# Optimization experiments

Measured on AMD Instinct MI355X. Metric: run time of the kernel, lower is better.

The kernel has to match this reference:

```python
import jax, jax.numpy as jnp
import numpy as np
import math

N, T, D, H = 64, 512, 1024, 1024

def setup_inputs() -> dict:
    key = jax.random.key(0)
    k1, k2, k3, k4 = jax.random.split(key, 4)
    x = jax.random.normal(k1, (N, T, D), dtype=jnp.float32)
    h0 = jax.random.normal(k2, (N, H), dtype=jnp.float32)
    Wx = jax.random.normal(k3, (D, 4 * H), dtype=jnp.float32) / math.sqrt(D)
    Wh = jax.random.normal(k4, (H, 4 * H), dtype=jnp.float32) / math.sqrt(H)
    b = jnp.zeros((4 * H,), dtype=jnp.float32)
    return {"x": x, "h0": h0, "Wx": Wx, "Wh": Wh, "b": b}

def reference(x, h0, Wx, Wh, b):
    Hdim = h0.shape[1]
    c0 = jnp.zeros_like(h0)
    # Precompute input projection for all timesteps: [N,T,4H] -> time-major [T,N,4H]
    xW = jnp.einsum('ntd,dk->tnk', x, Wx) + b

    def step(carry, xw_t):
        prev_h, prev_c = carry
        a = xw_t + prev_h @ Wh  # [N, 4H]
        i = jax.nn.sigmoid(a[:, :Hdim])
        f = jax.nn.sigmoid(a[:, Hdim:2 * Hdim])
        o = jax.nn.sigmoid(a[:, 2 * Hdim:3 * Hdim])
        g = jnp.tanh(a[:, 3 * Hdim:])
        next_c = f * prev_c + i * g
        next_h = o * jnp.tanh(next_c)
        return (next_h, next_c), next_h

    _, hs = jax.lax.scan(step, (h0, c0), xW)  # hs: [T, N, H]
    return jnp.transpose(hs, (1, 0, 2))  # [N, T, H]
```

## Files before the change

kernel.cpp:

```cpp
#include <hip/hip_runtime.h>

typedef short bf16x8 __attribute__((ext_vector_type(8)));
typedef float f32x4 __attribute__((ext_vector_type(4)));

static constexpr int kT = 512;
static constexpr int kN = 64;
static constexpr int kD = 1024;
static constexpr int kH = 1024;
static constexpr int kG = 4 * kH;

__device__ __forceinline__ unsigned short f2bf(float f) {
  unsigned u = __builtin_bit_cast(unsigned, f);
  return (unsigned short)((u + 0x7fffu + ((u >> 16) & 1u)) >> 16);
}
__device__ __forceinline__ unsigned pack2(float a, float b) {
  return (unsigned)f2bf(a) | ((unsigned)f2bf(b) << 16);
}
__device__ __forceinline__ float fsigmoid(float v) {
  return __builtin_amdgcn_rcpf(1.0f + __expf(-v));
}
__device__ __forceinline__ float ftanh(float v) {
  return 1.0f - 2.0f * __builtin_amdgcn_rcpf(__expf(2.0f * v) + 1.0f);
}

__device__ __forceinline__ bf16x8 gld16_coh(unsigned long long a) {
  bf16x8 r;
  asm volatile("global_load_dwordx4 %0, %1, off sc0 sc1" : "=v"(r) : "v"(a) : "memory");
  return r;
}
__device__ __forceinline__ bf16x8 gld16(unsigned long long a) {
  bf16x8 r;
  asm volatile("global_load_dwordx4 %0, %1, off" : "=v"(r) : "v"(a) : "memory");
  return r;
}

__global__ __launch_bounds__(256) void xconv(const float* __restrict__ x,
                                             unsigned short* __restrict__ xbf) {
  const int gid = blockIdx.x * 256 + threadIdx.x;
  const float4* x4 = (const float4*)x;
  uint4* o = (uint4*)xbf;
  for (int i = gid; i < (kN * kT * kD) / 8; i += 2048 * 256) {
    const float4 f0 = x4[2 * i];
    const float4 f1 = x4[2 * i + 1];
    uint4 p;
    p.x = pack2(f0.x, f0.y); p.y = pack2(f0.z, f0.w);
    p.z = pack2(f1.x, f1.y); p.w = pack2(f1.z, f1.w);
    o[i] = p;
  }
}

template <bool PRE>
__global__ __launch_bounds__(256, 1)
void lstm_fg(const float* __restrict__ x, const float* __restrict__ h0,
             const float* __restrict__ Wx, const float* __restrict__ Wh,
             const float* __restrict__ bias, float* __restrict__ out,
             unsigned short* __restrict__ hbuf, unsigned* __restrict__ flags,
             const unsigned short* __restrict__ xbf) {
  __shared__ float ps[2][16 * 320];

  const int tid = threadIdx.x;
  const int bx = blockIdx.x;
  const int dom = (bx & 7) >> 1;
  const int ug = ((bx >> 3) << 1) | (bx & 1);
  const int wv = tid >> 6;
  const int lane = tid & 63;

  const int colc = ug * 16 + (lane & 15);
  const int krow = (lane >> 4) * 8;
  const int kb = wv * 256;
  bf16x8 wxf[4][8], whf[4][8];
#pragma unroll
  for (int ct = 0; ct < 4; ++ct) {
#pragma unroll
    for (int ks = 0; ks < 8; ++ks) {
      bf16x8 vx, vh;
#pragma unroll
      for (int e = 0; e < 8; ++e) {
        const size_t k = (size_t)(kb + ks * 32 + krow + e);
        vx[e] = (short)f2bf(Wx[k * kG + ct * kH + colc]);
        vh[e] = (short)f2bf(Wh[k * kG + ct * kH + colc]);
      }
      wxf[ct][ks] = vx;
      whf[ct][ks] = vh;
    }
  }

  const int n_l = tid >> 4;
  const int j_l = tid & 15;
  const int jg = ug * 16 + j_l;
  const float b_i = bias[jg];
  const float b_f = bias[kH + jg];
  const float b_o = bias[2 * kH + jg];
  const float b_g = bias[3 * kH + jg];
  float c = 0.0f;

  const int arow = lane & 15;
  const int nrow = dom * 16 + arow;
  const unsigned long long xbase0 =
      (unsigned long long)nrow * kT * kD * 2 + (unsigned long long)(kb + krow) * 2;
  const unsigned long long hbase0 =
      (unsigned long long)nrow * kH * 2 + (unsigned long long)(kb + krow) * 2;
  const unsigned pubeidx = (unsigned)((dom * 16 + n_l) * kH + jg);

  unsigned* myflag = flags + (dom * 256 + ug * 4 + wv);
  unsigned* pollp = flags + (dom * 256 + wv * 64 + lane);

  bf16x8 xfrag[8], hfrag[8];

  if (PRE) {
    const unsigned long long xb = (unsigned long long)xbf + xbase0;
#pragma unroll
    for (int ks = 0; ks < 8; ++ks) xfrag[ks] = gld16(xb + (unsigned)(ks * 64));
    asm volatile("s_waitcnt vmcnt(0)" ::: "memory");
    __builtin_amdgcn_sched_barrier(0);
  } else {
    const float* xr = x + (size_t)nrow * kT * kD + (kb + krow);
#pragma unroll
    for (int ks = 0; ks < 8; ++ks) {
      const float4 f0 = *(const float4*)(xr + ks * 32);
      const float4 f1 = *(const float4*)(xr + ks * 32 + 4);
      bf16x8 v;
      v[0] = (short)f2bf(f0.x); v[1] = (short)f2bf(f0.y);
      v[2] = (short)f2bf(f0.z); v[3] = (short)f2bf(f0.w);
      v[4] = (short)f2bf(f1.x); v[5] = (short)f2bf(f1.y);
      v[6] = (short)f2bf(f1.z); v[7] = (short)f2bf(f1.w);
      xfrag[ks] = v;
    }
  }
  f32x4 acc[4];
#pragma unroll
  for (int ct = 0; ct < 4; ++ct) acc[ct] = (f32x4){0.f, 0.f, 0.f, 0.f};
#pragma unroll
  for (int ks = 0; ks < 8; ++ks)
#pragma unroll
    for (int ct = 0; ct < 4; ++ct)
      acc[ct] = __builtin_amdgcn_mfma_f32_16x16x32_bf16(xfrag[ks], wxf[ct][ks], acc[ct], 0, 0, 0);
  {
    const float* hr = h0 + (size_t)nrow * kH + (kb + krow);
#pragma unroll
    for (int ks = 0; ks < 8; ++ks) {
      const float4 f0 = *(const float4*)(hr + ks * 32);
      const float4 f1 = *(const float4*)(hr + ks * 32 + 4);
      bf16x8 v;
      v[0] = (short)f2bf(f0.x); v[1] = (short)f2bf(f0.y);
      v[2] = (short)f2bf(f0.z); v[3] = (short)f2bf(f0.w);
      v[4] = (short)f2bf(f1.x); v[5] = (short)f2bf(f1.y);
      v[6] = (short)f2bf(f1.z); v[7] = (short)f2bf(f1.w);
      hfrag[ks] = v;
    }
  }

  for (int t = 0; t < kT; ++t) {
    asm volatile("s_waitcnt vmcnt(4)" ::: "memory");
    __builtin_amdgcn_sched_barrier(0);
#pragma unroll
    for (int ks = 0; ks < 4; ++ks)
#pragma unroll
      for (int ct = 0; ct < 4; ++ct)
        acc[ct] = __builtin_amdgcn_mfma_f32_16x16x32_bf16(hfrag[ks], whf[ct][ks], acc[ct], 0, 0, 0);
    asm volatile("s_waitcnt vmcnt(0)" ::: "memory");
    __builtin_amdgcn_sched_barrier(0);
#pragma unroll
    for (int ks = 4; ks < 8; ++ks)
#pragma unroll
      for (int ct = 0; ct < 4; ++ct)
        acc[ct] = __builtin_amdgcn_mfma_f32_16x16x32_bf16(hfrag[ks], whf[ct][ks], acc[ct], 0, 0, 0);

    float* p = ps[t & 1];
#pragma unroll
    for (int ct = 0; ct < 4; ++ct)
      *(f32x4*)&p[(ct * 4 + wv) * 320 + (lane & 15) * 20 + (lane >> 4) * 4] = acc[ct];
    __syncthreads();

    float a4[4];
#pragma unroll
    for (int g = 0; g < 4; ++g) {
      a4[g] = p[(g * 4 + 0) * 320 + j_l * 20 + n_l]
            + p[(g * 4 + 1) * 320 + j_l * 20 + n_l]
            + p[(g * 4 + 2) * 320 + j_l * 20 + n_l]
            + p[(g * 4 + 3) * 320 + j_l * 20 + n_l];
    }
    const float gi = fsigmoid(a4[0] + b_i);
    const float gf = fsigmoid(a4[1] + b_f);
    const float go = fsigmoid(a4[2] + b_o);
    const float gg = ftanh(a4[3] + b_g);
    c = gf * c + gi * gg;
    const float hv = go * ftanh(c);

    if (t < kT - 1) {
      const unsigned tgt = (unsigned)(t + 1);
      const unsigned buf1 = tgt & 1;
      const unsigned mybf = (unsigned)f2bf(hv);
      const unsigned up = (unsigned)__shfl_xor((int)mybf, 1);
      if ((j_l & 1) == 0) {
        __hip_atomic_store((unsigned*)(hbuf + buf1 * (kN * kH) + pubeidx),
                           mybf | (up << 16), __ATOMIC_RELAXED, __HIP_MEMORY_SCOPE_AGENT);
      }
      asm volatile("s_waitcnt vmcnt(0)" ::: "memory");
      __builtin_amdgcn_sched_barrier(0);
      if (lane == 0)
        __hip_atomic_store(myflag, tgt, __ATOMIC_RELAXED, __HIP_MEMORY_SCOPE_AGENT);

      __builtin_nontemporal_store(hv, &out[((size_t)(dom * 16 + n_l) * kT + t) * kH + jg]);

      if (PRE) {
        const unsigned long long xb = (unsigned long long)xbf + xbase0 +
                                      (unsigned long long)(t + 1) * 2048u;
#pragma unroll
        for (int ks = 0; ks < 8; ++ks) xfrag[ks] = gld16(xb + (unsigned)(ks * 64));
        asm volatile("s_waitcnt vmcnt(0)" ::: "memory");
        __builtin_amdgcn_sched_barrier(0);
      } else {
        const float* xr = x + (size_t)nrow * kT * kD + (size_t)(t + 1) * kD + (kb + krow);
#pragma unroll
        for (int ks = 0; ks < 8; ++ks) {
          const float4 f0 = *(const float4*)(xr + ks * 32);
          const float4 f1 = *(const float4*)(xr + ks * 32 + 4);
          bf16x8 v;
          v[0] = (short)f2bf(f0.x); v[1] = (short)f2bf(f0.y);
          v[2] = (short)f2bf(f0.z); v[3] = (short)f2bf(f0.w);
          v[4] = (short)f2bf(f1.x); v[5] = (short)f2bf(f1.y);
          v[6] = (short)f2bf(f1.z); v[7] = (short)f2bf(f1.w);
          xfrag[ks] = v;
        }
      }
#pragma unroll
      for (int ct = 0; ct < 4; ++ct) acc[ct] = (f32x4){0.f, 0.f, 0.f, 0.f};
#pragma unroll
      for (int ks = 0; ks < 8; ++ks)
#pragma unroll
        for (int ct = 0; ct < 4; ++ct)
          acc[ct] = __builtin_amdgcn_mfma_f32_16x16x32_bf16(xfrag[ks], wxf[ct][ks], acc[ct], 0, 0, 0);

      for (;;) {
        const unsigned v = __hip_atomic_load(pollp, __ATOMIC_RELAXED,
                                             __HIP_MEMORY_SCOPE_AGENT);
        if (__all((int)v >= (int)tgt)) break;
        __builtin_amdgcn_s_sleep(1);
      }
      __builtin_amdgcn_sched_barrier(0);

      const unsigned long long hb = (unsigned long long)hbuf +
                                    (unsigned long long)buf1 * (kN * kH * 2) + hbase0;
#pragma unroll
      for (int ks = 0; ks < 8; ++ks) hfrag[ks] = gld16_coh(hb + (unsigned)(ks * 64));
    } else {
      __builtin_nontemporal_store(hv, &out[((size_t)(dom * 16 + n_l) * kT + t) * kH + jg]);
    }
  }
}

extern "C" void kernel_launch(void* const* d_in, const int* in_sizes, int n_in,
                              void* d_out, int out_size, void* d_ws, size_t ws_size,
                              hipStream_t stream) {
  (void)in_sizes; (void)n_in; (void)out_size;
  const float* x  = (const float*)d_in[0];
  const float* h0 = (const float*)d_in[1];
  const float* Wx = (const float*)d_in[2];
  const float* Wh = (const float*)d_in[3];
  const float* b  = (const float*)d_in[4];
  float* out = (float*)d_out;

  const size_t o_hbuf = 4096;
  const size_t o_xbf = o_hbuf + 262144;
  const size_t need_pre = o_xbf + (size_t)kN * kT * kD * 2;

  unsigned* flags = (unsigned*)d_ws;
  unsigned short* hbuf = (unsigned short*)((char*)d_ws + o_hbuf);
  unsigned short* xbf = (unsigned short*)((char*)d_ws + o_xbf);

  hipMemsetAsync(d_ws, 0, 4096, stream);

  if (ws_size >= need_pre) {
    hipLaunchKernelGGL(xconv, dim3(2048), dim3(256), 0, stream, x, xbf);
    hipLaunchKernelGGL(HIP_KERNEL_NAME(lstm_fg<true>), dim3(256), dim3(256), 0, stream,
                       x, h0, Wx, Wh, b, out, hbuf, flags, xbf);
  } else {
    hipLaunchKernelGGL(HIP_KERNEL_NAME(lstm_fg<false>), dim3(256), dim3(256), 0, stream,
                       x, h0, Wx, Wh, b, out, hbuf, flags,
                       (const unsigned short*)nullptr);
  }
}
```

Baseline: 2.011 ms.

## Replace flag-then-load handoff with timestep-tagged hidden-state words polled directly

Each published hidden value is now stored as a 32-bit word holding the timestep tag in the upper half and the bf16 value in the lower half. Consumers poll the data words themselves, removing the serial flag-poll-then-load round trip per step. The old flag path is kept as a fallback after a bounded number of polling attempts. This doubles hidden-state buffer traffic, issues 64 scalar atomic loads per lane per poll, and moves the flag store after the x prefetch.

After: 4.990 ms. 148% more time.

```diff
diff --git a/kernel.cpp b/kernel.cpp
--- a/kernel.cpp
+++ b/kernel.cpp
@@ -23,8 +23,8 @@
   return 1.0f - 2.0f * __builtin_amdgcn_rcpf(__expf(2.0f * v) + 1.0f);
 }
 
-__device__ __forceinline__ bf16x8 gld16_coh(unsigned long long a) {
-  bf16x8 r;
+__device__ __forceinline__ uint4 gld16_coh_u(unsigned long long a) {
+  uint4 r;
   asm volatile("global_load_dwordx4 %0, %1, off sc0 sc1" : "=v"(r) : "v"(a) : "memory");
   return r;
 }
@@ -51,10 +51,10 @@
 
 template <bool PRE>
 __global__ __launch_bounds__(256, 1)
-void lstm_fg(const float* __restrict__ x, const float* __restrict__ h0,
+void lstm_tf(const float* __restrict__ x, const float* __restrict__ h0,
              const float* __restrict__ Wx, const float* __restrict__ Wh,
              const float* __restrict__ bias, float* __restrict__ out,
-             unsigned short* __restrict__ hbuf, unsigned* __restrict__ flags,
+             unsigned* __restrict__ hTag, unsigned* __restrict__ flags,
              const unsigned short* __restrict__ xbf) {
   __shared__ float ps[2][16 * 320];
 
@@ -98,8 +98,7 @@
   const int nrow = dom * 16 + arow;
   const unsigned long long xbase0 =
       (unsigned long long)nrow * kT * kD * 2 + (unsigned long long)(kb + krow) * 2;
-  const unsigned long long hbase0 =
-      (unsigned long long)nrow * kH * 2 + (unsigned long long)(kb + krow) * 2;
+  const unsigned hrowelem = (unsigned)(nrow * kH + kb + krow);
   const unsigned pubeidx = (unsigned)((dom * 16 + n_l) * kH + jg);
 
   unsigned* myflag = flags + (dom * 256 + ug * 4 + wv);
@@ -151,17 +150,8 @@
   }
 
   for (int t = 0; t < kT; ++t) {
-    asm volatile("s_waitcnt vmcnt(4)" ::: "memory");
-    __builtin_amdgcn_sched_barrier(0);
-#pragma unroll
-    for (int ks = 0; ks < 4; ++ks)
-#pragma unroll
-      for (int ct = 0; ct < 4; ++ct)
-        acc[ct] = __builtin_amdgcn_mfma_f32_16x16x32_bf16(hfrag[ks], whf[ct][ks], acc[ct], 0, 0, 0);
-    asm volatile("s_waitcnt vmcnt(0)" ::: "memory");
-    __builtin_amdgcn_sched_barrier(0);
-#pragma unroll
-    for (int ks = 4; ks < 8; ++ks)
+#pragma unroll
+    for (int ks = 0; ks < 8; ++ks)
 #pragma unroll
       for (int ct = 0; ct < 4; ++ct)
         acc[ct] = __builtin_amdgcn_mfma_f32_16x16x32_bf16(hfrag[ks], whf[ct][ks], acc[ct], 0, 0, 0);
@@ -189,27 +179,16 @@
 
     if (t < kT - 1) {
       const unsigned tgt = (unsigned)(t + 1);
-      const unsigned buf1 = tgt & 1;
-      const unsigned mybf = (unsigned)f2bf(hv);
-      const unsigned up = (unsigned)__shfl_xor((int)mybf, 1);
-      if ((j_l & 1) == 0) {
-        __hip_atomic_store((unsigned*)(hbuf + buf1 * (kN * kH) + pubeidx),
-                           mybf | (up << 16), __ATOMIC_RELAXED, __HIP_MEMORY_SCOPE_AGENT);
-      }
-      asm volatile("s_waitcnt vmcnt(0)" ::: "memory");
-      __builtin_amdgcn_sched_barrier(0);
-      if (lane == 0)
-        __hip_atomic_store(myflag, tgt, __ATOMIC_RELAXED, __HIP_MEMORY_SCOPE_AGENT);
-
-      __builtin_nontemporal_store(hv, &out[((size_t)(dom * 16 + n_l) * kT + t) * kH + jg]);
+      unsigned* tbuf = hTag + (tgt & 1) * (unsigned)(kN * kH);
+
+      __hip_atomic_store(tbuf + pubeidx, (tgt << 16) | (unsigned)f2bf(hv),
+                         __ATOMIC_RELAXED, __HIP_MEMORY_SCOPE_AGENT);
 
       if (PRE) {
         const unsigned long long xb = (unsigned long long)xbf + xbase0 +
                                       (unsigned long long)(t + 1) * 2048u;
 #pragma unroll
         for (int ks = 0; ks < 8; ++ks) xfrag[ks] = gld16(xb + (unsigned)(ks * 64));
-        asm volatile("s_waitcnt vmcnt(0)" ::: "memory");
-        __builtin_amdgcn_sched_barrier(0);
       } else {
         const float* xr = x + (size_t)nrow * kT * kD + (size_t)(t + 1) * kD + (kb + krow);
 #pragma unroll
@@ -224,6 +203,13 @@
           xfrag[ks] = v;
         }
       }
+      asm volatile("s_waitcnt vmcnt(0)" ::: "memory");
+      __builtin_amdgcn_sched_barrier(0);
+      if (lane == 0)
+        __hip_atomic_store(myflag, tgt, __ATOMIC_RELAXED, __HIP_MEMORY_SCOPE_AGENT);
+
+      __builtin_nontemporal_store(hv, &out[((size_t)(dom * 16 + n_l) * kT + t) * kH + jg]);
+
 #pragma unroll
       for (int ct = 0; ct < 4; ++ct) acc[ct] = (f32x4){0.f, 0.f, 0.f, 0.f};
 #pragma unroll
@@ -232,18 +218,62 @@
         for (int ct = 0; ct < 4; ++ct)
           acc[ct] = __builtin_amdgcn_mfma_f32_16x16x32_bf16(xfrag[ks], wxf[ct][ks], acc[ct], 0, 0, 0);
 
-      for (;;) {
-        const unsigned v = __hip_atomic_load(pollp, __ATOMIC_RELAXED,
-                                             __HIP_MEMORY_SCOPE_AGENT);
-        if (__all((int)v >= (int)tgt)) break;
+      const unsigned* pb = tbuf + hrowelem;
+      unsigned tgv[8][8];
+      bool got = false;
+#pragma unroll 1
+      for (int it = 0; it < 24; ++it) {
+        unsigned bad = 0;
+#pragma unroll
+        for (int ks = 0; ks < 8; ++ks)
+#pragma unroll
+          for (int e = 0; e < 8; ++e) {
+            tgv[ks][e] = __hip_atomic_load(pb + ks * 32 + e, __ATOMIC_RELAXED,
+                                           __HIP_MEMORY_SCOPE_AGENT);
+            bad |= (tgv[ks][e] >> 16) ^ tgt;
+          }
+        if (__all(bad == 0)) { got = true; break; }
         __builtin_amdgcn_s_sleep(1);
       }
-      __builtin_amdgcn_sched_barrier(0);
-
-      const unsigned long long hb = (unsigned long long)hbuf +
-                                    (unsigned long long)buf1 * (kN * kH * 2) + hbase0;
-#pragma unroll
-      for (int ks = 0; ks < 8; ++ks) hfrag[ks] = gld16_coh(hb + (unsigned)(ks * 64));
+
+      if (got) {
+#pragma unroll
+        for (int ks = 0; ks < 8; ++ks) {
+          uint4 w;
+          w.x = (tgv[ks][0] & 0xFFFFu) | (tgv[ks][1] << 16);
+          w.y = (tgv[ks][2] & 0xFFFFu) | (tgv[ks][3] << 16);
+          w.z = (tgv[ks][4] & 0xFFFFu) | (tgv[ks][5] << 16);
+          w.w = (tgv[ks][6] & 0xFFFFu) | (tgv[ks][7] << 16);
+          hfrag[ks] = __builtin_bit_cast(bf16x8, w);
+        }
+      } else {
+        for (;;) {
+          const unsigned v = __hip_atomic_load(pollp, __ATOMIC_RELAXED,
+                                               __HIP_MEMORY_SCOPE_AGENT);
+          if (__all((int)v >= (int)tgt)) break;
+          __builtin_amdgcn_s_sleep(1);
+        }
+        __builtin_amdgcn_sched_barrier(0);
+        const unsigned long long hb = (unsigned long long)(tbuf + hrowelem);
+        uint4 tg4[16];
+#pragma unroll
+        for (int ks = 0; ks < 8; ++ks) {
+          tg4[2 * ks] = gld16_coh_u(hb + (unsigned)(ks * 128));
+          tg4[2 * ks + 1] = gld16_coh_u(hb + (unsigned)(ks * 128 + 16));
+        }
+        asm volatile("s_waitcnt vmcnt(0)" ::: "memory");
+        __builtin_amdgcn_sched_barrier(0);
+#pragma unroll
+        for (int ks = 0; ks < 8; ++ks) {
+          const uint4 a = tg4[2 * ks], b2 = tg4[2 * ks + 1];
+          uint4 w;
+          w.x = (a.x & 0xFFFFu) | (a.y << 16);
+          w.y = (a.z & 0xFFFFu) | (a.w << 16);
+          w.z = (b2.x & 0xFFFFu) | (b2.y << 16);
+          w.w = (b2.z & 0xFFFFu) | (b2.w << 16);
+          hfrag[ks] = __builtin_bit_cast(bf16x8, w);
+        }
+      }
     } else {
       __builtin_nontemporal_store(hv, &out[((size_t)(dom * 16 + n_l) * kT + t) * kH + jg]);
     }
@@ -261,23 +291,23 @@
   const float* b  = (const float*)d_in[4];
   float* out = (float*)d_out;
 
-  const size_t o_hbuf = 4096;
-  const size_t o_xbf = o_hbuf + 262144;
+  const size_t o_htag = 4096;
+  const size_t o_xbf = o_htag + 524288;
   const size_t need_pre = o_xbf + (size_t)kN * kT * kD * 2;
 
   unsigned* flags = (unsigned*)d_ws;
-  unsigned short* hbuf = (unsigned short*)((char*)d_ws + o_hbuf);
+  unsigned* hTag = (unsigned*)((char*)d_ws + o_htag);
   unsigned short* xbf = (unsigned short*)((char*)d_ws + o_xbf);
 
-  hipMemsetAsync(d_ws, 0, 4096, stream);
+  hipMemsetAsync(d_ws, 0, o_xbf, stream);
 
   if (ws_size >= need_pre) {
     hipLaunchKernelGGL(xconv, dim3(2048), dim3(256), 0, stream, x, xbf);
-    hipLaunchKernelGGL(HIP_KERNEL_NAME(lstm_fg<true>), dim3(256), dim3(256), 0, stream,
-                       x, h0, Wx, Wh, b, out, hbuf, flags, xbf);
+    hipLaunchKernelGGL(HIP_KERNEL_NAME(lstm_tf<true>), dim3(256), dim3(256), 0, stream,
+                       x, h0, Wx, Wh, b, out, hTag, flags, xbf);
   } else {
-    hipLaunchKernelGGL(HIP_KERNEL_NAME(lstm_fg<false>), dim3(256), dim3(256), 0, stream,
-                       x, h0, Wx, Wh, b, out, hbuf, flags,
+    hipLaunchKernelGGL(HIP_KERNEL_NAME(lstm_tf<false>), dim3(256), dim3(256), 0, stream,
+                       x, h0, Wx, Wh, b, out, hTag, flags,
                        (const unsigned short*)nullptr);
   }
 }
```

## Aggregate per-wave flags into one per-workgroup flag and pipeline h loads finer

Applied to the files above, without the earlier changes.

Each wave now bumps a shared-memory counter, and only the last wave of the workgroup publishes the step flag. This cuts the flag array from per-wave to per-workgroup entries, so pollers read 16 flags instead of 64. The wait on the hidden-state loads is split into four stages (vmcnt 6/4/2/0), letting MFMAs start as soon as each pair of fragments arrives. The flag publish now also waits for the x prefetch loads to finish, which may delay signalling. The unbounded shared counter relies on wave ordering across steps.

Result: slower. 2.688 ms (+33.7%).

```diff
diff --git a/kernel.cpp b/kernel.cpp
--- a/kernel.cpp
+++ b/kernel.cpp
@@ -33,6 +33,9 @@
   asm volatile("global_load_dwordx4 %0, %1, off" : "=v"(r) : "v"(a) : "memory");
   return r;
 }
+
+#define VMCNT(n) do { asm volatile("s_waitcnt vmcnt(" #n ")" ::: "memory"); \
+                      __builtin_amdgcn_sched_barrier(0); } while (0)
 
 __global__ __launch_bounds__(256) void xconv(const float* __restrict__ x,
                                              unsigned short* __restrict__ xbf) {
@@ -51,12 +54,13 @@
 
 template <bool PRE>
 __global__ __launch_bounds__(256, 1)
-void lstm_fg(const float* __restrict__ x, const float* __restrict__ h0,
-             const float* __restrict__ Wx, const float* __restrict__ Wh,
-             const float* __restrict__ bias, float* __restrict__ out,
-             unsigned short* __restrict__ hbuf, unsigned* __restrict__ flags,
-             const unsigned short* __restrict__ xbf) {
+void lstm_fg2(const float* __restrict__ x, const float* __restrict__ h0,
+              const float* __restrict__ Wx, const float* __restrict__ Wh,
+              const float* __restrict__ bias, float* __restrict__ out,
+              unsigned short* __restrict__ hbuf, unsigned* __restrict__ flags,
+              const unsigned short* __restrict__ xbf) {
   __shared__ float ps[2][16 * 320];
+  __shared__ unsigned wgcnt;
 
   const int tid = threadIdx.x;
   const int bx = blockIdx.x;
@@ -64,6 +68,8 @@
   const int ug = ((bx >> 3) << 1) | (bx & 1);
   const int wv = tid >> 6;
   const int lane = tid & 63;
+
+  if (tid == 0) wgcnt = 0;
 
   const int colc = ug * 16 + (lane & 15);
   const int krow = (lane >> 4) * 8;
@@ -102,8 +108,8 @@
       (unsigned long long)nrow * kH * 2 + (unsigned long long)(kb + krow) * 2;
   const unsigned pubeidx = (unsigned)((dom * 16 + n_l) * kH + jg);
 
-  unsigned* myflag = flags + (dom * 256 + ug * 4 + wv);
-  unsigned* pollp = flags + (dom * 256 + wv * 64 + lane);
+  unsigned* myflag = flags + (dom * 64 + ug);
+  unsigned* pollp = flags + (dom * 64 + wv * 16 + (lane & 15));
 
   bf16x8 xfrag[8], hfrag[8];
 
@@ -111,8 +117,7 @@
     const unsigned long long xb = (unsigned long long)xbf + xbase0;
 #pragma unroll
     for (int ks = 0; ks < 8; ++ks) xfrag[ks] = gld16(xb + (unsigned)(ks * 64));
-    asm volatile("s_waitcnt vmcnt(0)" ::: "memory");
-    __builtin_amdgcn_sched_barrier(0);
+    VMCNT(0);
   } else {
     const float* xr = x + (size_t)nrow * kT * kD + (kb + krow);
 #pragma unroll
@@ -149,19 +154,30 @@
       hfrag[ks] = v;
     }
   }
+  VMCNT(0);
 
   for (int t = 0; t < kT; ++t) {
-    asm volatile("s_waitcnt vmcnt(4)" ::: "memory");
-    __builtin_amdgcn_sched_barrier(0);
-#pragma unroll
-    for (int ks = 0; ks < 4; ++ks)
+    VMCNT(6);
+#pragma unroll
+    for (int ks = 0; ks < 2; ++ks)
 #pragma unroll
       for (int ct = 0; ct < 4; ++ct)
         acc[ct] = __builtin_amdgcn_mfma_f32_16x16x32_bf16(hfrag[ks], whf[ct][ks], acc[ct], 0, 0, 0);
-    asm volatile("s_waitcnt vmcnt(0)" ::: "memory");
-    __builtin_amdgcn_sched_barrier(0);
-#pragma unroll
-    for (int ks = 4; ks < 8; ++ks)
+    VMCNT(4);
+#pragma unroll
+    for (int ks = 2; ks < 4; ++ks)
+#pragma unroll
+      for (int ct = 0; ct < 4; ++ct)
+        acc[ct] = __builtin_amdgcn_mfma_f32_16x16x32_bf16(hfrag[ks], whf[ct][ks], acc[ct], 0, 0, 0);
+    VMCNT(2);
+#pragma unroll
+    for (int ks = 4; ks < 6; ++ks)
+#pragma unroll
+      for (int ct = 0; ct < 4; ++ct)
+        acc[ct] = __builtin_amdgcn_mfma_f32_16x16x32_bf16(hfrag[ks], whf[ct][ks], acc[ct], 0, 0, 0);
+    VMCNT(0);
+#pragma unroll
+    for (int ks = 6; ks < 8; ++ks)
 #pragma unroll
       for (int ct = 0; ct < 4; ++ct)
         acc[ct] = __builtin_amdgcn_mfma_f32_16x16x32_bf16(hfrag[ks], whf[ct][ks], acc[ct], 0, 0, 0);
@@ -190,27 +206,29 @@
     if (t < kT - 1) {
       const unsigned tgt = (unsigned)(t + 1);
       const unsigned buf1 = tgt & 1;
+
       const unsigned mybf = (unsigned)f2bf(hv);
       const unsigned up = (unsigned)__shfl_xor((int)mybf, 1);
       if ((j_l & 1) == 0) {
         __hip_atomic_store((unsigned*)(hbuf + buf1 * (kN * kH) + pubeidx),
                            mybf | (up << 16), __ATOMIC_RELAXED, __HIP_MEMORY_SCOPE_AGENT);
       }
-      asm volatile("s_waitcnt vmcnt(0)" ::: "memory");
-      __builtin_amdgcn_sched_barrier(0);
-      if (lane == 0)
-        __hip_atomic_store(myflag, tgt, __ATOMIC_RELAXED, __HIP_MEMORY_SCOPE_AGENT);
-
       __builtin_nontemporal_store(hv, &out[((size_t)(dom * 16 + n_l) * kT + t) * kH + jg]);
-
       if (PRE) {
         const unsigned long long xb = (unsigned long long)xbf + xbase0 +
                                       (unsigned long long)(t + 1) * 2048u;
 #pragma unroll
         for (int ks = 0; ks < 8; ++ks) xfrag[ks] = gld16(xb + (unsigned)(ks * 64));
-        asm volatile("s_waitcnt vmcnt(0)" ::: "memory");
-        __builtin_amdgcn_sched_barrier(0);
-      } else {
+      }
+      VMCNT(0);
+
+      if (lane == 0) {
+        const unsigned old = atomicAdd(&wgcnt, 1u);
+        if (old == 4u * t + 3u)
+          __hip_atomic_store(myflag, tgt, __ATOMIC_RELAXED, __HIP_MEMORY_SCOPE_AGENT);
+      }
+
+      if (!PRE) {
         const float* xr = x + (size_t)nrow * kT * kD + (size_t)(t + 1) * kD + (kb + krow);
 #pragma unroll
         for (int ks = 0; ks < 8; ++ks) {
@@ -273,10 +291,10 @@
 
   if (ws_size >= need_pre) {
     hipLaunchKernelGGL(xconv, dim3(2048), dim3(256), 0, stream, x, xbf);
-    hipLaunchKernelGGL(HIP_KERNEL_NAME(lstm_fg<true>), dim3(256), dim3(256), 0, stream,
+    hipLaunchKernelGGL(HIP_KERNEL_NAME(lstm_fg2<true>), dim3(256), dim3(256), 0, stream,
                        x, h0, Wx, Wh, b, out, hbuf, flags, xbf);
   } else {
-    hipLaunchKernelGGL(HIP_KERNEL_NAME(lstm_fg<false>), dim3(256), dim3(256), 0, stream,
+    hipLaunchKernelGGL(HIP_KERNEL_NAME(lstm_fg2<false>), dim3(256), dim3(256), 0, stream,
                        x, h0, Wx, Wh, b, out, hbuf, flags,
                        (const unsigned short*)nullptr);
   }
```
